# Performance work log

Hardware: AMD Instinct MI355X
Metric: run time of the kernel (lower is better)

The kernel has to match this reference:

```python
import jax, jax.numpy as jnp
import numpy as np

N_VOX = 200000   # active voxels
K = 27           # 3x3x3 kernel offsets
P = 100000       # rulebook pairs per kernel offset
C_IN = 64
C_OUT = 64
BN_EPS = 1e-5


def setup_inputs() -> dict:
    key = jax.random.key(0)
    k1, k2, k3, k4, k5 = jax.random.split(key, 5)
    features = jax.random.normal(k1, (N_VOX, C_IN), dtype=jnp.float32)
    weight = jax.random.normal(k2, (K, C_IN, C_OUT), dtype=jnp.float32) * 0.05
    bias = jax.random.normal(k3, (C_OUT,), dtype=jnp.float32) * 0.05
    gamma = jnp.ones((C_OUT,), dtype=jnp.float32)
    beta = jnp.zeros((C_OUT,), dtype=jnp.float32)
    in_idx = jax.random.randint(k4, (K, P), 0, N_VOX, dtype=jnp.int32)
    out_idx = jax.random.randint(k5, (K, P), 0, N_VOX, dtype=jnp.int32)
    return {"features": features, "weight": weight, "bias": bias,
            "gamma": gamma, "beta": beta, "in_idx": in_idx, "out_idx": out_idx}


def reference(features, weight, bias, gamma, beta, in_idx, out_idx):
    # --- sparse submanifold conv: gather -> per-offset GEMM -> scatter-add ---
    gathered = features[in_idx]                         # [K, P, C_in]
    partial = jnp.einsum('kpc,kcd->kpd', gathered, weight)  # [K, P, C_out]
    out = jnp.zeros((N_VOX, C_OUT), dtype=features.dtype)
    out = out.at[out_idx.reshape(-1)].add(partial.reshape(-1, C_OUT))
    out = out + bias                                    # conv bias
    # --- BatchNorm1d (training mode: batch stats, biased variance) ---
    mean = jnp.mean(out, axis=0)
    var = jnp.mean(jnp.square(out - mean), axis=0)
    normed = (out - mean) * jax.lax.rsqrt(var + BN_EPS) * gamma + beta
    # --- ReLU ---
    return jnp.maximum(normed, 0.0)
```

## Files before the change

kernel.cpp:

```cpp
#include <hip/hip_runtime.h>
#include <hip/hip_bf16.h>

#define N_VOX 200000
#define KOFF 27
#define PPK 100000
#define C 64
#define BN_EPS 1e-5f

typedef __bf16 bf16x8 __attribute__((ext_vector_type(8)));
typedef __bf16 bf16x4 __attribute__((ext_vector_type(4)));
typedef float f32x4 __attribute__((ext_vector_type(4)));

__global__ __launch_bounds__(256)
void convert_features(const float* __restrict__ f, __bf16* __restrict__ fb)
{
    const size_t total4 = (size_t)N_VOX * C / 4;
    const size_t i = (size_t)blockIdx.x * blockDim.x + threadIdx.x;
    if (i >= total4) return;
    const float4 v = ((const float4*)f)[i];
    bf16x4 o;
    o.x = (__bf16)v.x; o.y = (__bf16)v.y; o.z = (__bf16)v.z; o.w = (__bf16)v.w;
    ((bf16x4*)fb)[i] = o;
}

__global__ __launch_bounds__(256)
void convert_weight(const float* __restrict__ w, __bf16* __restrict__ wt)
{
    const int k = blockIdx.x;
    const float* W = w + (size_t)k * C * C;
    __bf16* Wt = wt + (size_t)k * C * C;
    for (int idx = threadIdx.x; idx < C * C; idx += 256) {
        const int ci = idx >> 6, co = idx & 63;
        Wt[co * C + ci] = (__bf16)W[idx];
    }
}

__global__ __launch_bounds__(256)
void hist_kernel(const int* __restrict__ out_idx, unsigned* __restrict__ counts,
                 unsigned* __restrict__ slot, int k0, int npair)
{
    const int i = blockIdx.x * 256 + threadIdx.x;
    if (i < npair) {
        const int o = out_idx[(size_t)k0 * PPK + i];
        slot[i] = atomicAdd(&counts[o], 1u);
    }
}

__global__ __launch_bounds__(256)
void scan1(unsigned* __restrict__ counts, unsigned* __restrict__ offsets,
           unsigned* __restrict__ bsums)
{
    __shared__ unsigned sdata[256];
    const int t = threadIdx.x;
    const int base = blockIdx.x * 1024 + t * 4;
    unsigned v[4]; unsigned s = 0;
#pragma unroll
    for (int u = 0; u < 4; ++u) {
        const bool ok = (base + u < N_VOX);
        v[u] = ok ? counts[base + u] : 0u;
        if (ok) counts[base + u] = 0u;
        s += v[u];
    }
    sdata[t] = s;
    __syncthreads();
    for (int off = 1; off < 256; off <<= 1) {
        const unsigned add = (t >= off) ? sdata[t - off] : 0u;
        __syncthreads();
        sdata[t] += add;
        __syncthreads();
    }
    const unsigned incl = sdata[t];
    unsigned run = incl - s;
    if (t == 255) bsums[blockIdx.x] = incl;
#pragma unroll
    for (int u = 0; u < 4; ++u) {
        if (base + u < N_VOX) offsets[base + u] = run;
        run += v[u];
    }
}

__global__ __launch_bounds__(256)
void scan2(unsigned* __restrict__ bsums, int nb)
{
    __shared__ unsigned sdata[256];
    const int t = threadIdx.x;
    const unsigned s = (t < nb) ? bsums[t] : 0u;
    sdata[t] = s;
    __syncthreads();
    for (int off = 1; off < 256; off <<= 1) {
        const unsigned add = (t >= off) ? sdata[t - off] : 0u;
        __syncthreads();
        sdata[t] += add;
        __syncthreads();
    }
    if (t < nb) bsums[t] = sdata[t] - s;
}

__global__ __launch_bounds__(256)
void scan3(unsigned* __restrict__ offsets, const unsigned* __restrict__ bsums)
{
    const int i = blockIdx.x * 256 + threadIdx.x;
    if (i < N_VOX) offsets[i] += bsums[i >> 10];
}

__global__ __launch_bounds__(256)
void slot_fill(const int* __restrict__ out_idx,
               const unsigned* __restrict__ offsets,
               unsigned* __restrict__ slot, int k0, int npair)
{
    const int i = blockIdx.x * 256 + threadIdx.x;
    if (i < npair) {
        const int o = out_idx[(size_t)k0 * PPK + i];
        slot[i] += offsets[o];
    }
}

__global__ __launch_bounds__(256)
void conv_scatter(const __bf16* __restrict__ featb, const __bf16* __restrict__ wtb,
                  const int* __restrict__ in_idx, const unsigned* __restrict__ slot,
                  __bf16* __restrict__ partial, int k0)
{
    constexpr int TP = 256;
    __shared__ __bf16 sA[TP * 64];

    const int kloc = blockIdx.y;
    const int k = k0 + kloc;
    const int tile_base = blockIdx.x * TP;
    const int t = threadIdx.x;
    const int lane = t & 63;
    const int wave = t >> 6;
    const int m16 = lane & 15;
    const int quad = lane >> 4;

    unsigned my_slot = 0u;
    {
        const int pair = tile_base + t;
        if (pair < PPK) my_slot = slot[(size_t)kloc * PPK + pair];
    }

    const __bf16* Wt = wtb + (size_t)k * C * C;
    bf16x8 bfrag[4][2];
#pragma unroll
    for (int nt = 0; nt < 4; ++nt)
#pragma unroll
        for (int kc = 0; kc < 2; ++kc)
            bfrag[nt][kc] = *(const bf16x8*)(Wt + (nt * 16 + m16) * C + kc * 32 + quad * 8);

    const int c8 = t & 7;
    const int r0 = t >> 3;
#pragma unroll
    for (int it = 0; it < 8; ++it) {
        const int r = r0 + it * 32;
        const int pair = tile_base + r;
        const int row = (pair < PPK) ? in_idx[(size_t)k * PPK + pair] : 0;
        const float4 v = *(const float4*)(featb + (size_t)row * C + c8 * 8);
        *(float4*)(sA + r * 64 + ((c8 ^ (r0 & 7)) << 3)) = v;
    }
    __syncthreads();

    f32x4 acc[4][4] = {};
    const int mbase = wave * 64;
#pragma unroll
    for (int kc = 0; kc < 2; ++kc) {
        bf16x8 afrag[4];
#pragma unroll
        for (int mt = 0; mt < 4; ++mt)
            afrag[mt] = *(const bf16x8*)(sA + (mbase + mt * 16 + m16) * 64
                                         + ((((kc << 2) | quad) ^ (m16 & 7)) << 3));
#pragma unroll
        for (int nt = 0; nt < 4; ++nt)
#pragma unroll
            for (int mt = 0; mt < 4; ++mt)
                acc[mt][nt] = __builtin_amdgcn_mfma_f32_16x16x32_bf16(
                    afrag[mt], bfrag[nt][kc], acc[mt][nt], 0, 0, 0);
    }

#pragma unroll
    for (int mt = 0; mt < 4; ++mt) {
#pragma unroll
        for (int reg = 0; reg < 4; ++reg) {
            const int rloc = mt * 16 + quad * 4 + reg;
            const unsigned s = __shfl(my_slot, rloc, 64);
            const int pair = tile_base + mbase + rloc;
            if (pair < PPK) {
                bf16x4 pv;
                pv.x = (__bf16)acc[mt][0][reg];
                pv.y = (__bf16)acc[mt][1][reg];
                pv.z = (__bf16)acc[mt][2][reg];
                pv.w = (__bf16)acc[mt][3][reg];
                *(bf16x4*)(partial + (size_t)s * C + (m16 << 2)) = pv;
            }
        }
    }
}

__global__ __launch_bounds__(256)
void reduce_kernel(const __bf16* __restrict__ partial,
                   const unsigned* __restrict__ offsets,
                   float* __restrict__ out, const int first, const unsigned np)
{
    const int wave = threadIdx.x >> 6;
    const int lane = threadIdx.x & 63;
    const int e = lane >> 4;
    const int j = lane & 15;
    const int stride = gridDim.x * 4;
    for (int o = blockIdx.x * 4 + wave; o < N_VOX; o += stride) {
        const unsigned beg = offsets[o];
        const unsigned end = (o + 1 < N_VOX) ? offsets[o + 1] : np;
        float a0 = 0.f, a1 = 0.f, a2 = 0.f, a3 = 0.f;
        for (unsigned s = beg + e; s < end; s += 4) {
            const bf16x4 v = *(const bf16x4*)(partial + (size_t)s * C + (j << 2));
            a0 += (float)v.x; a1 += (float)v.y; a2 += (float)v.z; a3 += (float)v.w;
        }
#pragma unroll
        for (int mask = 16; mask <= 32; mask <<= 1) {
            a0 += __shfl_xor(a0, mask, 64);
            a1 += __shfl_xor(a1, mask, 64);
            a2 += __shfl_xor(a2, mask, 64);
            a3 += __shfl_xor(a3, mask, 64);
        }
        if (e == 0) {
            float* orow = out + (size_t)o * C;
            if (first) {
                orow[j] = a0; orow[16 + j] = a1; orow[32 + j] = a2; orow[48 + j] = a3;
            } else {
                orow[j] += a0; orow[16 + j] += a1; orow[32 + j] += a2; orow[48 + j] += a3;
            }
        }
    }
}

__global__ __launch_bounds__(256)
void conv_mfma(const __bf16* __restrict__ featb, const __bf16* __restrict__ wtb,
               const int* __restrict__ in_idx, const int* __restrict__ out_idx,
               float* __restrict__ out)
{
    constexpr int TP = 256;
    constexpr int STRIDE = 72;
    __shared__ __bf16 sA[TP * STRIDE];
    __shared__ int s_out[TP];

    const int k = blockIdx.y;
    const int tile_base = blockIdx.x * TP;
    const int t = threadIdx.x;
    const int lane = t & 63;
    const int wave = t >> 6;
    const int m16 = lane & 15;
    const int quad = lane >> 4;

    const __bf16* Wt = wtb + (size_t)k * C * C;
    bf16x8 bfrag[4][2];
#pragma unroll
    for (int nt = 0; nt < 4; ++nt)
#pragma unroll
        for (int kc = 0; kc < 2; ++kc)
            bfrag[nt][kc] = *(const bf16x8*)(Wt + (nt * 16 + m16) * C + kc * 32 + quad * 8);

    {
        const int pair = tile_base + t;
        s_out[t] = (pair < PPK) ? out_idx[(size_t)k * PPK + pair] : 0;
    }

    const int c8 = t & 7;
    const int r0 = t >> 3;
#pragma unroll
    for (int it = 0; it < 8; ++it) {
        const int r = r0 + it * 32;
        const int pair = tile_base + r;
        const int row = (pair < PPK) ? in_idx[(size_t)k * PPK + pair] : 0;
        const float4 v = *(const float4*)(featb + (size_t)row * C + c8 * 8);
        *(float4*)(sA + r * STRIDE + c8 * 8) = v;
    }
    __syncthreads();

    f32x4 acc[4][4] = {};
    const int mbase = wave * 64;
#pragma unroll
    for (int kc = 0; kc < 2; ++kc) {
        bf16x8 afrag[4];
#pragma unroll
        for (int mt = 0; mt < 4; ++mt)
            afrag[mt] = *(const bf16x8*)(sA + (mbase + mt * 16 + m16) * STRIDE + kc * 32 + quad * 8);
#pragma unroll
        for (int nt = 0; nt < 4; ++nt)
#pragma unroll
            for (int mt = 0; mt < 4; ++mt)
                acc[mt][nt] = __builtin_amdgcn_mfma_f32_16x16x32_bf16(
                    afrag[mt], bfrag[nt][kc], acc[mt][nt], 0, 0, 0);
    }

#pragma unroll
    for (int mt = 0; mt < 4; ++mt) {
#pragma unroll
        for (int reg = 0; reg < 4; ++reg) {
            const int r = mbase + mt * 16 + quad * 4 + reg;
            const int pair = tile_base + r;
            if (pair < PPK) {
                const int o = s_out[r];
                float* orow = out + (size_t)o * C + m16;
#pragma unroll
                for (int nt = 0; nt < 4; ++nt)
                    unsafeAtomicAdd(orow + nt * 16, acc[mt][nt][reg]);
            }
        }
    }
}

__global__ __launch_bounds__(256)
void stats_kernel(const float* __restrict__ out,
                  float* __restrict__ stats,
                  int rows_per_block)
{
    __shared__ float ssum[256];
    __shared__ float ssq[256];
    const int c   = threadIdx.x & 63;
    const int sub = threadIdx.x >> 6;
    const int row0 = blockIdx.x * rows_per_block;
    const int row1 = min(row0 + rows_per_block, N_VOX);
    float s = 0.f, q = 0.f;
    for (int r = row0 + sub; r < row1; r += 4) {
        const float v = out[(size_t)r * C + c];
        s += v;
        q += v * v;
    }
    ssum[threadIdx.x] = s;
    ssq[threadIdx.x]  = q;
    __syncthreads();
    if (sub == 0) {
        s = ssum[c] + ssum[64 + c] + ssum[128 + c] + ssum[192 + c];
        q = ssq[c]  + ssq[64 + c]  + ssq[128 + c]  + ssq[192 + c];
        unsafeAtomicAdd(&stats[c], s);
        unsafeAtomicAdd(&stats[64 + c], q);
    }
}

__global__ void finalize_params(const float* __restrict__ stats,
                                const float* __restrict__ gamma,
                                const float* __restrict__ beta,
                                float* __restrict__ ss)
{
    const int c = threadIdx.x;
    const float inv_n = 1.0f / (float)N_VOX;
    const float mean  = stats[c] * inv_n;
    const float var   = stats[64 + c] * inv_n - mean * mean;
    const float scale = rsqrtf(var + BN_EPS) * gamma[c];
    ss[c]      = scale;
    ss[64 + c] = beta[c] - mean * scale;
}

__global__ __launch_bounds__(256)
void norm_kernel(float* __restrict__ out, const float* __restrict__ ss)
{
    const size_t total4 = (size_t)N_VOX * C / 4;
    const size_t idx = (size_t)blockIdx.x * blockDim.x + threadIdx.x;
    if (idx >= total4) return;
    const int c4 = (int)(idx & 15);
    float4 v = ((const float4*)out)[idx];
    const float4 sc = ((const float4*)ss)[c4];
    const float4 sh = ((const float4*)(ss + 64))[c4];
    v.x = fmaxf(v.x * sc.x + sh.x, 0.f);
    v.y = fmaxf(v.y * sc.y + sh.y, 0.f);
    v.z = fmaxf(v.z * sc.z + sh.z, 0.f);
    v.w = fmaxf(v.w * sc.w + sh.w, 0.f);
    ((float4*)out)[idx] = v;
}

static inline size_t align_up(size_t x) { return (x + 255) & ~(size_t)255; }

extern "C" void kernel_launch(void* const* d_in, const int* in_sizes, int n_in,
                              void* d_out, int out_size, void* d_ws, size_t ws_size,
                              hipStream_t stream)
{
    const float* features = (const float*)d_in[0];
    const float* weight   = (const float*)d_in[1];
    const float* gamma    = (const float*)d_in[3];
    const float* beta     = (const float*)d_in[4];
    const int*   in_idx   = (const int*)d_in[5];
    const int*   out_idx  = (const int*)d_in[6];
    float* out = (float*)d_out;

    char* base = (char*)d_ws;
    size_t off = 0;
    __bf16* featb = (__bf16*)(base + off); off += align_up((size_t)N_VOX * C * 2);
    __bf16* wtb   = (__bf16*)(base + off); off += align_up((size_t)KOFF * C * C * 2);
    float*  stats = (float*)(base + off);  off += align_up(128 * 4);
    float*  ss    = (float*)(base + off);  off += align_up(128 * 4);
    unsigned* counts  = (unsigned*)(base + off); off += align_up((size_t)N_VOX * 4);
    unsigned* offsets = (unsigned*)(base + off); off += align_up((size_t)N_VOX * 4);
    unsigned* bsums   = (unsigned*)(base + off); off += align_up(256 * 4);
    const size_t fixed = off;

    int g_cap = 0;
    if (ws_size > fixed)
        g_cap = (int)((ws_size - fixed) / ((size_t)PPK * 132));
    if (g_cap > KOFF) g_cap = KOFF;

    hipMemsetAsync(stats, 0, 128 * sizeof(float), stream);

    const size_t total4 = (size_t)N_VOX * C / 4;
    convert_features<<<(int)((total4 + 255) / 256), 256, 0, stream>>>(features, featb);
    convert_weight<<<KOFF, 256, 0, stream>>>(weight, wtb);

    if (g_cap >= 2) {
        const int G = (KOFF + g_cap - 1) / g_cap;
        const int gmax = (KOFF + G - 1) / G;
        unsigned* slot = (unsigned*)(base + off);
        __bf16* partial = (__bf16*)(base + off + align_up((size_t)gmax * PPK * 4));
        const int gbase_sz = KOFF / G, rem = KOFF % G;
        hipMemsetAsync(counts, 0, (size_t)N_VOX * 4, stream);
        int k0 = 0;
        for (int ci = 0; ci < G; ++ci) {
            const int g = gbase_sz + (ci < rem ? 1 : 0);
            const int np = g * PPK;
            hist_kernel<<<(np + 255) / 256, 256, 0, stream>>>(out_idx, counts, slot, k0, np);
            scan1<<<(N_VOX + 1023) / 1024, 256, 0, stream>>>(counts, offsets, bsums);
            scan2<<<1, 256, 0, stream>>>(bsums, (N_VOX + 1023) / 1024);
            scan3<<<(N_VOX + 255) / 256, 256, 0, stream>>>(offsets, bsums);
            slot_fill<<<(np + 255) / 256, 256, 0, stream>>>(out_idx, offsets, slot, k0, np);
            dim3 cgrid((PPK + 255) / 256, g);
            conv_scatter<<<cgrid, 256, 0, stream>>>(featb, wtb, in_idx, slot, partial, k0);
            reduce_kernel<<<1024, 256, 0, stream>>>(partial, offsets, out,
                                                    ci == 0 ? 1 : 0, (unsigned)np);
            k0 += g;
        }
    } else {
        hipMemsetAsync(out, 0, (size_t)N_VOX * C * sizeof(float), stream);
        dim3 cgrid((PPK + 255) / 256, KOFF);
        conv_mfma<<<cgrid, 256, 0, stream>>>(featb, wtb, in_idx, out_idx, out);
    }

    const int rpb = (N_VOX + 511) / 512;
    stats_kernel<<<512, 256, 0, stream>>>(out, stats, rpb);

    finalize_params<<<1, 64, 0, stream>>>(stats, gamma, beta, ss);

    norm_kernel<<<(int)((total4 + 255) / 256), 256, 0, stream>>>(out, ss);
}
```

Measured before the change: 660.6 us.

## Fuse scan, slot fill, BN stats and finalize into neighbouring kernels

Several small passes are folded into neighbouring kernels. The counts/stats memsets move into convert_weight, scan2+scan3 become one kernel where each block recomputes its prefix from bsums, and slot_fill is dropped by computing the slot inside conv_scatter from rank+offsets. The stats pass becomes a per-block reduction with atomics in the final reduce_kernel, and finalize_params is folded into norm_kernel. This removes launches and one full read of the output in exchange for redundant per-block prefix sums, extra per-thread BN parameter math, and atomic float accumulation order.

```diff
diff --git a/kernel.cpp b/kernel.cpp
--- a/kernel.cpp
+++ b/kernel.cpp
@@ -24,7 +24,9 @@
 }
 
 __global__ __launch_bounds__(256)
-void convert_weight(const float* __restrict__ w, __bf16* __restrict__ wt)
+void convert_weight(const float* __restrict__ w, __bf16* __restrict__ wt,
+                    unsigned* __restrict__ counts_or_null,
+                    float* __restrict__ stats)
 {
     const int k = blockIdx.x;
     const float* W = w + (size_t)k * C * C;
@@ -33,16 +35,21 @@
         const int ci = idx >> 6, co = idx & 63;
         Wt[co * C + ci] = (__bf16)W[idx];
     }
+    if (counts_or_null) {
+        for (int i = blockIdx.x * 256 + threadIdx.x; i < N_VOX; i += KOFF * 256)
+            counts_or_null[i] = 0u;
+        if (blockIdx.x == 0 && threadIdx.x < 128) stats[threadIdx.x] = 0.f;
+    }
 }
 
 __global__ __launch_bounds__(256)
 void hist_kernel(const int* __restrict__ out_idx, unsigned* __restrict__ counts,
-                 unsigned* __restrict__ slot, int k0, int npair)
+                 unsigned* __restrict__ rank, int k0, int npair)
 {
     const int i = blockIdx.x * 256 + threadIdx.x;
     if (i < npair) {
         const int o = out_idx[(size_t)k0 * PPK + i];
-        slot[i] = atomicAdd(&counts[o], 1u);
+        rank[i] = atomicAdd(&counts[o], 1u);
     }
 }
 
@@ -80,44 +87,22 @@
 }
 
 __global__ __launch_bounds__(256)
-void scan2(unsigned* __restrict__ bsums, int nb)
-{
-    __shared__ unsigned sdata[256];
-    const int t = threadIdx.x;
-    const unsigned s = (t < nb) ? bsums[t] : 0u;
-    sdata[t] = s;
-    __syncthreads();
-    for (int off = 1; off < 256; off <<= 1) {
-        const unsigned add = (t >= off) ? sdata[t - off] : 0u;
-        __syncthreads();
-        sdata[t] += add;
-        __syncthreads();
-    }
-    if (t < nb) bsums[t] = sdata[t] - s;
-}
-
-__global__ __launch_bounds__(256)
-void scan3(unsigned* __restrict__ offsets, const unsigned* __restrict__ bsums)
+void scan23(unsigned* __restrict__ offsets, const unsigned* __restrict__ bsums)
 {
     const int i = blockIdx.x * 256 + threadIdx.x;
-    if (i < N_VOX) offsets[i] += bsums[i >> 10];
-}
-
-__global__ __launch_bounds__(256)
-void slot_fill(const int* __restrict__ out_idx,
-               const unsigned* __restrict__ offsets,
-               unsigned* __restrict__ slot, int k0, int npair)
-{
-    const int i = blockIdx.x * 256 + threadIdx.x;
-    if (i < npair) {
-        const int o = out_idx[(size_t)k0 * PPK + i];
-        slot[i] += offsets[o];
-    }
+    const int q = blockIdx.x >> 2;
+    const int lane = threadIdx.x & 63;
+    unsigned s = 0;
+    for (int j = lane; j < q; j += 64) s += bsums[j];
+#pragma unroll
+    for (int m = 1; m < 64; m <<= 1) s += __shfl_xor(s, m, 64);
+    if (i < N_VOX) offsets[i] += s;
 }
 
 __global__ __launch_bounds__(256)
 void conv_scatter(const __bf16* __restrict__ featb, const __bf16* __restrict__ wtb,
-                  const int* __restrict__ in_idx, const unsigned* __restrict__ slot,
+                  const int* __restrict__ in_idx, const int* __restrict__ out_idx,
+                  const unsigned* __restrict__ rank, const unsigned* __restrict__ offsets,
                   __bf16* __restrict__ partial, int k0)
 {
     constexpr int TP = 256;
@@ -135,7 +120,10 @@
     unsigned my_slot = 0u;
     {
         const int pair = tile_base + t;
-        if (pair < PPK) my_slot = slot[(size_t)kloc * PPK + pair];
+        if (pair < PPK) {
+            const int o = out_idx[(size_t)k * PPK + pair];
+            my_slot = rank[(size_t)kloc * PPK + pair] + offsets[o];
+        }
     }
 
     const __bf16* Wt = wtb + (size_t)k * C * C;
@@ -197,13 +185,17 @@
 __global__ __launch_bounds__(256)
 void reduce_kernel(const __bf16* __restrict__ partial,
                    const unsigned* __restrict__ offsets,
-                   float* __restrict__ out, const int first, const unsigned np)
-{
+                   float* __restrict__ out, float* __restrict__ stats,
+                   const int first, const int last, const unsigned np)
+{
+    __shared__ float sstat[512];
     const int wave = threadIdx.x >> 6;
     const int lane = threadIdx.x & 63;
     const int e = lane >> 4;
     const int j = lane & 15;
     const int stride = gridDim.x * 4;
+    float t0 = 0.f, t1 = 0.f, t2 = 0.f, t3 = 0.f;
+    float q0 = 0.f, q1 = 0.f, q2 = 0.f, q3 = 0.f;
     for (int o = blockIdx.x * 4 + wave; o < N_VOX; o += stride) {
         const unsigned beg = offsets[o];
         const unsigned end = (o + 1 < N_VOX) ? offsets[o + 1] : np;
@@ -221,11 +213,36 @@
         }
         if (e == 0) {
             float* orow = out + (size_t)o * C;
-            if (first) {
-                orow[j] = a0; orow[16 + j] = a1; orow[32 + j] = a2; orow[48 + j] = a3;
-            } else {
-                orow[j] += a0; orow[16 + j] += a1; orow[32 + j] += a2; orow[48 + j] += a3;
+            if (!first) {
+                a0 += orow[j]; a1 += orow[16 + j]; a2 += orow[32 + j]; a3 += orow[48 + j];
             }
+            orow[j] = a0; orow[16 + j] = a1; orow[32 + j] = a2; orow[48 + j] = a3;
+            if (last) {
+                t0 += a0; q0 += a0 * a0;
+                t1 += a1; q1 += a1 * a1;
+                t2 += a2; q2 += a2 * a2;
+                t3 += a3; q3 += a3 * a3;
+            }
+        }
+    }
+    if (last) {
+        if (e == 0) {
+            sstat[wave * 64 + j]            = t0;
+            sstat[wave * 64 + 16 + j]       = t1;
+            sstat[wave * 64 + 32 + j]       = t2;
+            sstat[wave * 64 + 48 + j]       = t3;
+            sstat[256 + wave * 64 + j]      = q0;
+            sstat[256 + wave * 64 + 16 + j] = q1;
+            sstat[256 + wave * 64 + 32 + j] = q2;
+            sstat[256 + wave * 64 + 48 + j] = q3;
+        }
+        __syncthreads();
+        const int t = threadIdx.x;
+        if (t < 64) {
+            const float ss = sstat[t] + sstat[64 + t] + sstat[128 + t] + sstat[192 + t];
+            const float qq = sstat[256 + t] + sstat[320 + t] + sstat[384 + t] + sstat[448 + t];
+            unsafeAtomicAdd(&stats[t], ss);
+            unsafeAtomicAdd(&stats[64 + t], qq);
         }
     }
 }
@@ -334,34 +351,40 @@
     }
 }
 
-__global__ void finalize_params(const float* __restrict__ stats,
-                                const float* __restrict__ gamma,
-                                const float* __restrict__ beta,
-                                float* __restrict__ ss)
-{
-    const int c = threadIdx.x;
-    const float inv_n = 1.0f / (float)N_VOX;
-    const float mean  = stats[c] * inv_n;
-    const float var   = stats[64 + c] * inv_n - mean * mean;
-    const float scale = rsqrtf(var + BN_EPS) * gamma[c];
-    ss[c]      = scale;
-    ss[64 + c] = beta[c] - mean * scale;
-}
-
-__global__ __launch_bounds__(256)
-void norm_kernel(float* __restrict__ out, const float* __restrict__ ss)
+__global__ __launch_bounds__(256)
+void norm_kernel(float* __restrict__ out, const float* __restrict__ stats,
+                 const float* __restrict__ gamma, const float* __restrict__ beta)
 {
     const size_t total4 = (size_t)N_VOX * C / 4;
     const size_t idx = (size_t)blockIdx.x * blockDim.x + threadIdx.x;
     if (idx >= total4) return;
     const int c4 = (int)(idx & 15);
+    const float inv_n = 1.0f / (float)N_VOX;
+    const float4 sm = ((const float4*)stats)[c4];
+    const float4 sq = ((const float4*)(stats + 64))[c4];
+    const float4 g  = ((const float4*)gamma)[c4];
+    const float4 be = ((const float4*)beta)[c4];
     float4 v = ((const float4*)out)[idx];
-    const float4 sc = ((const float4*)ss)[c4];
-    const float4 sh = ((const float4*)(ss + 64))[c4];
-    v.x = fmaxf(v.x * sc.x + sh.x, 0.f);
-    v.y = fmaxf(v.y * sc.y + sh.y, 0.f);
-    v.z = fmaxf(v.z * sc.z + sh.z, 0.f);
-    v.w = fmaxf(v.w * sc.w + sh.w, 0.f);
+    {
+        const float mean = sm.x * inv_n;
+        const float sc = rsqrtf(sq.x * inv_n - mean * mean + BN_EPS) * g.x;
+        v.x = fmaxf(v.x * sc + (be.x - mean * sc), 0.f);
+    }
+    {
+        const float mean = sm.y * inv_n;
+        const float sc = rsqrtf(sq.y * inv_n - mean * mean + BN_EPS) * g.y;
+        v.y = fmaxf(v.y * sc + (be.y - mean * sc), 0.f);
+    }
+    {
+        const float mean = sm.z * inv_n;
+        const float sc = rsqrtf(sq.z * inv_n - mean * mean + BN_EPS) * g.z;
+        v.z = fmaxf(v.z * sc + (be.z - mean * sc), 0.f);
+    }
+    {
+        const float mean = sm.w * inv_n;
+        const float sc = rsqrtf(sq.w * inv_n - mean * mean + BN_EPS) * g.w;
+        v.w = fmaxf(v.w * sc + (be.w - mean * sc), 0.f);
+    }
     ((float4*)out)[idx] = v;
 }
 
@@ -389,50 +412,50 @@
     unsigned* offsets = (unsigned*)(base + off); off += align_up((size_t)N_VOX * 4);
     unsigned* bsums   = (unsigned*)(base + off); off += align_up(256 * 4);
     const size_t fixed = off;
+    (void)ss;
 
     int g_cap = 0;
     if (ws_size > fixed)
         g_cap = (int)((ws_size - fixed) / ((size_t)PPK * 132));
     if (g_cap > KOFF) g_cap = KOFF;
 
-    hipMemsetAsync(stats, 0, 128 * sizeof(float), stream);
+    const bool fused = (g_cap >= 2);
 
     const size_t total4 = (size_t)N_VOX * C / 4;
     convert_features<<<(int)((total4 + 255) / 256), 256, 0, stream>>>(features, featb);
-    convert_weight<<<KOFF, 256, 0, stream>>>(weight, wtb);
-
-    if (g_cap >= 2) {
+    convert_weight<<<KOFF, 256, 0, stream>>>(weight, wtb,
+                                             fused ? counts : nullptr, stats);
+
+    if (fused) {
         const int G = (KOFF + g_cap - 1) / g_cap;
         const int gmax = (KOFF + G - 1) / G;
-        unsigned* slot = (unsigned*)(base + off);
+        unsigned* rank = (unsigned*)(base + off);
         __bf16* partial = (__bf16*)(base + off + align_up((size_t)gmax * PPK * 4));
         const int gbase_sz = KOFF / G, rem = KOFF % G;
-        hipMemsetAsync(counts, 0, (size_t)N_VOX * 4, stream);
         int k0 = 0;
         for (int ci = 0; ci < G; ++ci) {
             const int g = gbase_sz + (ci < rem ? 1 : 0);
             const int np = g * PPK;
-            hist_kernel<<<(np + 255) / 256, 256, 0, stream>>>(out_idx, counts, slot, k0, np);
+            hist_kernel<<<(np + 255) / 256, 256, 0, stream>>>(out_idx, counts, rank, k0, np);
             scan1<<<(N_VOX + 1023) / 1024, 256, 0, stream>>>(counts, offsets, bsums);
-            scan2<<<1, 256, 0, stream>>>(bsums, (N_VOX + 1023) / 1024);
-            scan3<<<(N_VOX + 255) / 256, 256, 0, stream>>>(offsets, bsums);
-            slot_fill<<<(np + 255) / 256, 256, 0, stream>>>(out_idx, offsets, slot, k0, np);
+            scan23<<<(N_VOX + 255) / 256, 256, 0, stream>>>(offsets, bsums);
             dim3 cgrid((PPK + 255) / 256, g);
-            conv_scatter<<<cgrid, 256, 0, stream>>>(featb, wtb, in_idx, slot, partial, k0);
-            reduce_kernel<<<1024, 256, 0, stream>>>(partial, offsets, out,
-                                                    ci == 0 ? 1 : 0, (unsigned)np);
+            conv_scatter<<<cgrid, 256, 0, stream>>>(featb, wtb, in_idx, out_idx,
+                                                    rank, offsets, partial, k0);
+            reduce_kernel<<<1024, 256, 0, stream>>>(partial, offsets, out, stats,
+                                                    ci == 0 ? 1 : 0,
+                                                    ci == G - 1 ? 1 : 0,
+                                                    (unsigned)np);
             k0 += g;
         }
     } else {
+        hipMemsetAsync(stats, 0, 128 * sizeof(float), stream);
         hipMemsetAsync(out, 0, (size_t)N_VOX * C * sizeof(float), stream);
         dim3 cgrid((PPK + 255) / 256, KOFF);
         conv_mfma<<<cgrid, 256, 0, stream>>>(featb, wtb, in_idx, out_idx, out);
-    }
-
-    const int rpb = (N_VOX + 511) / 512;
-    stats_kernel<<<512, 256, 0, stream>>>(out, stats, rpb);
-
-    finalize_params<<<1, 64, 0, stream>>>(stats, gamma, beta, ss);
-
-    norm_kernel<<<(int)((total4 + 255) / 256), 256, 0, stream>>>(out, ss);
-}
+        const int rpb = (N_VOX + 511) / 512;
+        stats_kernel<<<512, 256, 0, stream>>>(out, stats, rpb);
+    }
+
+    norm_kernel<<<(int)((total4 + 255) / 256), 256, 0, stream>>>(out, stats, gamma, beta);
+}
```

Result: faster. 627.5 us (-5.0%).
